# Optimization experiments

Measured on AMD Instinct MI355X. Metric: run time of the kernel, lower is better.

The kernel has to match this reference:

```python
import jax, jax.numpy as jnp
import numpy as np

S, M, B, D, H, DH = 1024, 1024, 4, 1024, 16, 64
T = S + M


def _rel_shift(x):
    # x: [i, j, b, n] -> Transformer-XL relative shift
    i, j = x.shape[0], x.shape[1]
    zero_pad = jnp.zeros((i, 1) + x.shape[2:], x.dtype)
    x_padded = jnp.concatenate([zero_pad, x], axis=1)
    x_padded = x_padded.reshape((j + 1, i) + x.shape[2:])
    return x_padded[1:].reshape(x.shape)


def setup_inputs() -> dict:
    key = jax.random.key(0)
    ks = jax.random.split(key, 8)
    sc = 0.02
    x = jax.random.normal(ks[0], (S, B, D), jnp.float32)
    memory = jax.random.normal(ks[1], (M, B, D), jnp.float32)
    pos_emb = jax.random.normal(ks[2], (T, D), jnp.float32)
    pos_bias_u = jax.random.normal(ks[3], (H, DH), jnp.float32) * sc
    pos_bias_v = jax.random.normal(ks[4], (H, DH), jnp.float32) * sc
    W_qkv = jax.random.normal(ks[5], (D, 3 * H * DH), jnp.float32) * sc
    W_rel = jax.random.normal(ks[6], (D, H * DH), jnp.float32) * sc
    W_o = jax.random.normal(ks[7], (H * DH, D), jnp.float32) * sc
    gamma = jnp.ones((D,), jnp.float32)
    beta = jnp.zeros((D,), jnp.float32)
    # causal mask accounting for memory: query i attends keys j <= i + M
    causal = jnp.arange(T)[None, :] > (jnp.arange(S)[:, None] + M)
    mask = jnp.broadcast_to(causal[:, :, None], (S, T, B))
    return {"x": x, "pos_emb": pos_emb, "pos_bias_u": pos_bias_u,
            "pos_bias_v": pos_bias_v, "memory": memory,
            "W_qkv": W_qkv, "W_rel": W_rel, "W_o": W_o,
            "gamma": gamma, "beta": beta, "mask": mask}


def reference(x, pos_emb, pos_bias_u, pos_bias_v, memory, W_qkv, W_rel, W_o, gamma, beta, mask):
    seq_len, batch, d_model = x.shape
    num_head, d_head = pos_bias_u.shape
    scale = 1.0 / d_head ** 0.5

    c = jnp.concatenate([memory, x], axis=0)          # [T, B, D]
    total_len = c.shape[0]

    qkv = c @ W_qkv                                   # [T, B, 3*H*DH]
    q, k, v = jnp.split(qkv, 3, axis=-1)
    q = q.reshape(total_len, batch, num_head, d_head)[-seq_len:]  # [S,B,H,DH]
    k = k.reshape(total_len, batch, num_head, d_head)             # [T,B,H,DH]
    v = v.reshape(total_len, batch, num_head, d_head)             # [T,B,H,DH]
    r = (pos_emb @ W_rel).reshape(total_len, num_head, d_head)    # [T,H,DH]

    AC = jnp.einsum('ibnd,jbnd->ijbn', q + pos_bias_u, k)  # content-content
    BD = jnp.einsum('ibnd,jnd->ijbn', q + pos_bias_v, r)   # content-position
    BD = _rel_shift(BD)

    attn_score = (AC + BD) * scale                    # [S,T,B,H]
    attn_score = jnp.where(mask[:, :, :, None], -jnp.inf, attn_score)
    attn_prob = jax.nn.softmax(attn_score, axis=1)

    attn_vec = jnp.einsum('ijbn,jbnd->ibnd', attn_prob, v)
    attn_vec = attn_vec.reshape(seq_len, batch, num_head * d_head)
    attn_out = attn_vec @ W_o                         # [S,B,D]

    y = x + attn_out
    mu = jnp.mean(y, axis=-1, keepdims=True)
    var = jnp.var(y, axis=-1, keepdims=True)
    return (y - mu) / jnp.sqrt(var + 1e-5) * gamma + beta
```

## Files before the change

### kernel.cpp

```cpp
#include <hip/hip_runtime.h>
#include <math.h>
#include <cstdint>
#include <cstddef>


typedef _Float16 half_t;
typedef _Float16 half8 __attribute__((ext_vector_type(8)));
typedef _Float16 half4v __attribute__((ext_vector_type(4)));
typedef float f32x4 __attribute__((ext_vector_type(4)));

#define S_LEN 1024
#define M_LEN 1024
#define T_LEN 2048
#define BATCH 4
#define NHEAD 16

__device__ inline void async_copy16(const half_t* g, half_t* l) {
  __builtin_amdgcn_global_load_lds(
      (const __attribute__((address_space(1))) void*)g,
      (__attribute__((address_space(3))) void*)l, 16, 0, 0);
}

__global__ __launch_bounds__(256) void k_convert3(const float* __restrict__ mem,
                                                  const float* __restrict__ x,
                                                  const float* __restrict__ pos,
                                                  half_t* __restrict__ cbf,
                                                  half_t* __restrict__ posb) {
  const int i = blockIdx.x * 256 + threadIdx.x;
  const float* src;
  half_t* dst;
  int off;
  if (i < 1048576)      { src = mem; dst = cbf;           off = i; }
  else if (i < 2097152) { src = x;   dst = cbf + 4194304; off = i - 1048576; }
  else                  { src = pos; dst = posb;          off = i - 2097152; }
  const float4 v = ((const float4*)src)[off];
  half4v h;
  h[0] = (half_t)v.x; h[1] = (half_t)v.y; h[2] = (half_t)v.z; h[3] = (half_t)v.w;
  ((half4v*)dst)[off] = h;
}

__global__ __launch_bounds__(256) void k_transpose_w3(const float* __restrict__ Wqkv,
                                                      const float* __restrict__ Wrel,
                                                      const float* __restrict__ Wo,
                                                      half_t* __restrict__ wqkvT,
                                                      half_t* __restrict__ wrelT,
                                                      half_t* __restrict__ woT) {
  __shared__ float tile[64][65];
  const int y = blockIdx.y;
  const float* src; half_t* dst; int C, c0;
  if (y < 48)      { src = Wqkv; dst = wqkvT; C = 3072; c0 = y * 64; }
  else if (y < 64) { src = Wrel; dst = wrelT; C = 1024; c0 = (y - 48) * 64; }
  else             { src = Wo;   dst = woT;   C = 1024; c0 = (y - 64) * 64; }
  const int t = threadIdx.x;
  const int r0 = blockIdx.x * 64;
  const int tx = t & 63, ty4 = t >> 6;
#pragma unroll
  for (int k = 0; k < 16; ++k) {
    int row = k * 4 + ty4;
    tile[row][tx] = src[(size_t)(r0 + row) * C + c0 + tx];
  }
  __syncthreads();
#pragma unroll
  for (int k = 0; k < 16; ++k) {
    int orow = k * 4 + ty4;
    dst[(size_t)(c0 + orow) * 1024 + r0 + tx] = (half_t)tile[tx][orow];
  }
}

__device__ inline void gemm_body(const half_t* __restrict__ A,
                                 const half_t* __restrict__ B,
                                 half_t* __restrict__ C,
                                 int N, int K, int ld, int m0, int n0,
                                 half_t (*ldsA)[64], half_t (*ldsB)[64]) {
  const int t = threadIdx.x;
  const int wave = t >> 6, lane = t & 63, quad = lane >> 4, l15 = lane & 15;
  const int wm = (wave >> 1) * 64, wn = (wave & 1) * 64;
  const int srow = lane >> 3;
  const int scol = ((lane & 7) ^ srow) * 8;
  f32x4 acc[4][4] = {};
  for (int k0 = 0; k0 < K; k0 += 64) {
    __syncthreads();
#pragma unroll
    for (int i = 0; i < 4; ++i) {
      const int r0 = (wave * 4 + i) * 8;
      async_copy16(&A[(size_t)(m0 + r0 + srow) * ld + k0 + scol], &ldsA[r0][0]);
      async_copy16(&B[(size_t)(n0 + r0 + srow) * ld + k0 + scol], &ldsB[r0][0]);
    }
    __syncthreads();
#pragma unroll
    for (int ks = 0; ks < 2; ++ks) {
      half8 af[4], bf[4];
#pragma unroll
      for (int mt = 0; mt < 4; ++mt)
        af[mt] = *(const half8*)&ldsA[wm + mt * 16 + l15][((ks * 4 + quad) ^ (l15 & 7)) * 8];
#pragma unroll
      for (int nt = 0; nt < 4; ++nt)
        bf[nt] = *(const half8*)&ldsB[wn + nt * 16 + l15][((ks * 4 + quad) ^ (l15 & 7)) * 8];
#pragma unroll
      for (int mt = 0; mt < 4; ++mt)
#pragma unroll
        for (int nt = 0; nt < 4; ++nt)
          acc[mt][nt] = __builtin_amdgcn_mfma_f32_16x16x32_f16(af[mt], bf[nt], acc[mt][nt], 0, 0, 0);
    }
  }
#pragma unroll
  for (int mt = 0; mt < 4; ++mt)
#pragma unroll
    for (int nt = 0; nt < 4; ++nt)
#pragma unroll
      for (int r = 0; r < 4; ++r) {
        const int row = m0 + wm + mt * 16 + quad * 4 + r;
        const int col = n0 + wn + nt * 16 + l15;
        C[(size_t)row * N + col] = (half_t)acc[mt][nt][r];
      }
}

__global__ __launch_bounds__(256) void k_gemm_qkv_pos(const half_t* __restrict__ cbf,
                                                      const half_t* __restrict__ wqkvT,
                                                      half_t* __restrict__ qkv,
                                                      const half_t* __restrict__ posb,
                                                      const half_t* __restrict__ wrelT,
                                                      half_t* __restrict__ rb) {
  __shared__ half_t ldsA[128][64];
  __shared__ half_t ldsB[128][64];
  const int bid = blockIdx.x;
  if (bid < 1536)
    gemm_body(cbf, wqkvT, qkv, 3072, 1024, 1024, (bid & 63) * 128, (bid >> 6) * 128, ldsA, ldsB);
  else {
    const int b2 = bid - 1536;
    gemm_body(posb, wrelT, rb, 1024, 1024, 1024, (b2 & 15) * 128, (b2 >> 4) * 128, ldsA, ldsB);
  }
}

__global__ __launch_bounds__(256) void k_gemm_proj(const half_t* __restrict__ av,
                                                   const half_t* __restrict__ woT,
                                                   half_t* __restrict__ out0,
                                                   half_t* __restrict__ out1) {
  __shared__ half_t ldsA[128][64];
  __shared__ half_t ldsB[128][64];
  const int bid = blockIdx.x;
  const int h = bid >> 8, b2 = bid & 255;
  gemm_body(av + h * 512, woT + h * 512, h ? out1 : out0,
            1024, 512, 1024, (b2 & 31) * 128, (b2 >> 5) * 128, ldsA, ldsB);
}

__global__ __launch_bounds__(256) void k_transpose_v(const half_t* __restrict__ qkv,
                                                     half_t* __restrict__ vT) {
  __shared__ half_t tile[64][72];
  const int t = threadIdx.x;
  const int t0 = blockIdx.x * 64, bn = blockIdx.y, b = bn >> 4, n = bn & 15;
#pragma unroll
  for (int i = 0; i < 2; ++i) {
    const int ci = t + i * 256;
    const int row = ci >> 3, co = (ci & 7) * 8;
    *(half8*)&tile[row][co] =
        *(const half8*)&qkv[((size_t)(t0 + row) * BATCH + b) * 3072 + 2048 + n * 64 + co];
  }
  __syncthreads();
#pragma unroll
  for (int i = 0; i < 2; ++i) {
    const int ci = t + i * 256;
    const int dh = ci >> 3, to = (ci & 7) * 8;
    half8 v;
#pragma unroll
    for (int j = 0; j < 8; ++j) v[j] = tile[to + j][dh];
    *(half8*)&vT[((size_t)bn * 64 + dh) * 2048 + t0 + to] = v;
  }
}

__global__ __launch_bounds__(512, 4) void k_attn(const half_t* __restrict__ qkv,
                                                 const half_t* __restrict__ rbuf,
                                                 const half_t* __restrict__ vT,
                                                 const float* __restrict__ pbu,
                                                 const float* __restrict__ pbv,
                                                 half_t* __restrict__ av) {
  __shared__ __align__(16) half_t ldsK[64][64];
  __shared__ __align__(16) half_t ldsV[64][64];
  __shared__ __align__(16) half_t ldsR[256][64];
  __shared__ __align__(16) half_t ldsP[8][16][72];
  const int t = threadIdx.x;
  const int wave = t >> 6, lane = t & 63, quad = lane >> 4, l15 = lane & 15;

  const int li = blockIdx.x + 8 * blockIdx.y;
  const int c = li & 255, kr = li >> 8;
  const int xe = kr == 0 ? (c & 7) : 7 - (c & 7);
  const int bn = (c >> 3) + (kr << 5);
  const int i0 = xe * 128;
  const int b = bn >> 4, n = bn & 15;
  const int i_base = i0 + wave * 16;
  const int p0 = 896 - i0;

  half8 qu[2], qv[2];
#pragma unroll
  for (int ks = 0; ks < 2; ++ks) {
    const int dh0 = ks * 32 + quad * 8;
    const half8 qf = *(const half8*)&qkv[((size_t)(M_LEN + i_base + l15) * BATCH + b) * 3072 + n * 64 + dh0];
#pragma unroll
    for (int j = 0; j < 8; ++j) {
      const float qj = (float)qf[j];
      qu[ks][j] = (half_t)(qj + pbu[n * 64 + dh0 + j]);
      qv[ks][j] = (half_t)(qj + pbv[n * 64 + dh0 + j]);
    }
  }

  int bperm_idx[4];
  bool lo_sel[4];
#pragma unroll
  for (int r = 0; r < 4; ++r) {
    const int irow = quad * 4 + r;
    bperm_idx[r] = ((lane & 48) | ((l15 + 15 - irow) & 15)) << 2;
    lo_sel[r] = (l15 <= irow);
  }

  f32x4 oacc[4] = {};
  float lpart[4] = {0.f, 0.f, 0.f, 0.f};
  const float k1 = 0.125f * 1.44269504088896f;
  const float kC = -4.0f * 1.44269504088896f;

  const int srow = t >> 3, sc3 = t & 7;
  const int sxk = (sc3 ^ (srow & 7)) * 8;

  const int ntile = xe * 2 + 18;

  half8 kreg = *(const half8*)&qkv[((size_t)srow * BATCH + b) * 3072 + 1024 + n * 64 + sc3 * 8];
  half8 vreg = *(const half8*)&vT[((size_t)bn * 64 + srow) * 2048 + sc3 * 8];
  half8 rreg4[4];
  int rr4[4], rc4[4];
#pragma unroll
  for (int i = 0; i < 4; ++i) {
    const int ci = t + 512 * i;
    rr4[i] = ci >> 3; rc4[i] = ci & 7;
    const int ps = p0 + rr4[i] > 2047 ? 2047 : p0 + rr4[i];
    rreg4[i] = *(const half8*)&rbuf[(size_t)ps * 1024 + n * 64 + rc4[i] * 8];
  }
  half8 rpre;

  for (int kt = 0; kt < ntile; ++kt) {
    const int j0 = kt * 64;

    __syncthreads();
    *(half8*)&ldsK[srow][sxk] = kreg;
    *(half8*)&ldsV[srow][sxk] = vreg;
    if (kt == 0) {
#pragma unroll
      for (int i = 0; i < 4; ++i) {
        const int pg = p0 + rr4[i];
        *(half8*)&ldsR[pg & 255][(rc4[i] ^ (pg & 7)) * 8] = rreg4[i];
      }
    } else {
      const int pw = j0 + p0 + 192 + srow;
      *(half8*)&ldsR[pw & 255][(sc3 ^ (pw & 7)) * 8] = rpre;
    }
    __syncthreads();

    if (kt + 1 < ntile) {
      const int j0n = j0 + 64;
      kreg = *(const half8*)&qkv[((size_t)(j0n + srow) * BATCH + b) * 3072 + 1024 + n * 64 + sc3 * 8];
      vreg = *(const half8*)&vT[((size_t)bn * 64 + srow) * 2048 + j0n + sc3 * 8];
      const int pn = j0 + p0 + 256 + srow;
      const int pc = pn > 2047 ? 2047 : pn;
      rpre = *(const half8*)&rbuf[(size_t)pc * 1024 + n * 64 + sc3 * 8];
    }

    f32x4 ac[4] = {};
#pragma unroll
    for (int ks = 0; ks < 2; ++ks)
#pragma unroll
      for (int nt = 0; nt < 4; ++nt) {
        const int row = nt * 16 + l15;
        const half8 kf = *(const half8*)&ldsK[row][((ks * 4 + quad) ^ (row & 7)) * 8];
        ac[nt] = __builtin_amdgcn_mfma_f32_16x16x32_f16(qu[ks], kf, ac[nt], 0, 0, 0);
      }

    const int rbg = j0 + p0 + 112 - wave * 16;
    f32x4 ea[5] = {};
#pragma unroll
    for (int ks = 0; ks < 2; ++ks)
#pragma unroll
      for (int et = 0; et < 5; ++et) {
        const int pr = rbg + et * 16 + l15;
        const half8 rf = *(const half8*)&ldsR[pr & 255][((ks * 4 + quad) ^ (pr & 7)) * 8];
        ea[et] = __builtin_amdgcn_mfma_f32_16x16x32_f16(qv[ks], rf, ea[et], 0, 0, 0);
      }

    const bool maskt = j0 > i_base + 960;
#pragma unroll
    for (int r = 0; r < 4; ++r) {
      const int irow = quad * 4 + r;
      const int ig = i_base + irow;
      float rot[5];
#pragma unroll
      for (int et = 0; et < 5; ++et)
        rot[et] = __int_as_float(
            __builtin_amdgcn_ds_bpermute(bperm_idx[r], __float_as_int(ea[et][r])));
      float psum = 0.f;
#pragma unroll
      for (int nt = 0; nt < 4; ++nt) {
        const float ev = lo_sel[r] ? rot[nt] : rot[nt + 1];
        const int cj = nt * 16 + l15;
        float p = __builtin_amdgcn_exp2f(fmaf(ac[nt][r] + ev, k1, kC));
        if (maskt && (j0 + cj > ig + M_LEN)) p = 0.f;
        psum += p;
        ldsP[wave][irow][cj] = (half_t)p;
      }
      lpart[r] += psum;
    }
    __builtin_amdgcn_wave_barrier();

    half8 pa[2];
#pragma unroll
    for (int ks = 0; ks < 2; ++ks)
      pa[ks] = *(const half8*)&ldsP[wave][l15][ks * 32 + quad * 8];
#pragma unroll
    for (int ks = 0; ks < 2; ++ks)
#pragma unroll
      for (int dnt = 0; dnt < 4; ++dnt) {
        const int row = dnt * 16 + l15;
        const half8 vf = *(const half8*)&ldsV[row][((ks * 4 + quad) ^ (row & 7)) * 8];
        oacc[dnt] = __builtin_amdgcn_mfma_f32_16x16x32_f16(pa[ks], vf, oacc[dnt], 0, 0, 0);
      }
  }

#pragma unroll
  for (int r = 0; r < 4; ++r) {
    float l = lpart[r];
#pragma unroll
    for (int off = 1; off < 16; off <<= 1) l += __shfl_xor(l, off);
    const float inv = 1.0f / l;
    const int ig = i_base + quad * 4 + r;
#pragma unroll
    for (int dnt = 0; dnt < 4; ++dnt)
      av[((size_t)ig * BATCH + b) * 1024 + n * 64 + dnt * 16 + l15] = (half_t)(oacc[dnt][r] * inv);
  }
}

__global__ __launch_bounds__(256) void k_ln(const float* __restrict__ x,
                                            const half_t* __restrict__ ao0,
                                            const half_t* __restrict__ ao1,
                                            const float* __restrict__ gamma,
                                            const float* __restrict__ beta,
                                            float* __restrict__ out) {
  const int row = blockIdx.x;
  const int t = threadIdx.x;
  const float4 xv = ((const float4*)(x + (size_t)row * 1024))[t];
  const half4v a4 = ((const half4v*)(ao0 + (size_t)row * 1024))[t];
  const half4v b4 = ((const half4v*)(ao1 + (size_t)row * 1024))[t];
  const float y0 = xv.x + (float)a4[0] + (float)b4[0];
  const float y1 = xv.y + (float)a4[1] + (float)b4[1];
  const float y2 = xv.z + (float)a4[2] + (float)b4[2];
  const float y3 = xv.w + (float)a4[3] + (float)b4[3];
  float s = y0 + y1 + y2 + y3;
  float ss = y0 * y0 + y1 * y1 + y2 * y2 + y3 * y3;
#pragma unroll
  for (int off = 1; off < 64; off <<= 1) {
    s += __shfl_xor(s, off);
    ss += __shfl_xor(ss, off);
  }
  __shared__ float sb[4], ssb[4];
  if ((t & 63) == 0) { sb[t >> 6] = s; ssb[t >> 6] = ss; }
  __syncthreads();
  s = sb[0] + sb[1] + sb[2] + sb[3];
  ss = ssb[0] + ssb[1] + ssb[2] + ssb[3];
  const float mean = s * (1.f / 1024.f);
  const float var = ss * (1.f / 1024.f) - mean * mean;
  const float rstd = rsqrtf(var + 1e-5f);
  const float4 g = ((const float4*)gamma)[t];
  const float4 be = ((const float4*)beta)[t];
  float4 o;
  o.x = (y0 - mean) * rstd * g.x + be.x;
  o.y = (y1 - mean) * rstd * g.y + be.y;
  o.z = (y2 - mean) * rstd * g.z + be.z;
  o.w = (y3 - mean) * rstd * g.w + be.w;
  ((float4*)(out + (size_t)row * 1024))[t] = o;
}

extern "C" void kernel_launch(void* const* d_in, const int* in_sizes, int n_in,
                              void* d_out, int out_size, void* d_ws, size_t ws_size,
                              hipStream_t stream) {
  const float* x     = (const float*)d_in[0];
  const float* pos   = (const float*)d_in[1];
  const float* pbu   = (const float*)d_in[2];
  const float* pbv   = (const float*)d_in[3];
  const float* mem   = (const float*)d_in[4];
  const float* Wqkv  = (const float*)d_in[5];
  const float* Wrel  = (const float*)d_in[6];
  const float* Wo    = (const float*)d_in[7];
  const float* gamma = (const float*)d_in[8];
  const float* beta  = (const float*)d_in[9];
  float* out = (float*)d_out;

  half_t* ws    = (half_t*)d_ws;
  half_t* cbf   = ws;
  half_t* posb  = cbf + 8388608;
  half_t* wqkvT = posb + 2097152;
  half_t* wrelT = wqkvT + 3145728;
  half_t* woT   = wrelT + 1048576;
  half_t* qkv   = woT + 1048576;
  half_t* rb    = qkv + 25165824;
  half_t* vT    = rb + 2097152;
  half_t* av    = vT + 8388608;
  half_t* aout0 = qkv;
  half_t* aout1 = qkv + 4194304;

  k_convert3<<<10240, 256, 0, stream>>>(mem, x, pos, cbf, posb);
  k_transpose_w3<<<dim3(16, 80), 256, 0, stream>>>(Wqkv, Wrel, Wo, wqkvT, wrelT, woT);
  k_gemm_qkv_pos<<<1664, 256, 0, stream>>>(cbf, wqkvT, qkv, posb, wrelT, rb);
  k_transpose_v<<<dim3(32, 64), 256, 0, stream>>>(qkv, vT);
  k_attn<<<dim3(8, 64), 512, 0, stream>>>(qkv, rb, vT, pbu, pbv, av);
  k_gemm_proj<<<512, 256, 0, stream>>>(av, woT, aout0, aout1);
  k_ln<<<4096, 256, 0, stream>>>(x, aout0, aout1, gamma, beta, out);
}
```

Before: 333.4 us.

## Split attention key range into two balanced passes per block with combine kernel

Each attention block now handles two query tiles instead of one. It processes the first half of the key range for query tile kq and the second half for query tile 7-kq, so every block runs the same number of key tiles. This removes the causal-length imbalance between blocks. Because the softmax uses a fixed offset rather than a running max, partial outputs and row sums can be written unnormalized and added in a new small combine kernel. The cost is extra global writes and reads for the partial results, one more kernel launch, and a second Q/R prologue per block.

```diff
diff --git a/kernel.cpp b/kernel.cpp
--- a/kernel.cpp
+++ b/kernel.cpp
@@ -173,7 +173,9 @@
                                                  const half_t* __restrict__ vT,
                                                  const float* __restrict__ pbu,
                                                  const float* __restrict__ pbv,
-                                                 half_t* __restrict__ av) {
+                                                 half_t* __restrict__ av0,
+                                                 half_t* __restrict__ av1,
+                                                 float* __restrict__ lsum) {
   __shared__ __align__(16) half_t ldsK[64][64];
   __shared__ __align__(16) half_t ldsV[64][64];
   __shared__ __align__(16) half_t ldsR[256][64];
@@ -182,26 +184,9 @@
   const int wave = t >> 6, lane = t & 63, quad = lane >> 4, l15 = lane & 15;
 
   const int li = blockIdx.x + 8 * blockIdx.y;
-  const int c = li & 255, kr = li >> 8;
-  const int xe = kr == 0 ? (c & 7) : 7 - (c & 7);
-  const int bn = (c >> 3) + (kr << 5);
-  const int i0 = xe * 128;
+  const int kq = li & 7;
+  const int bn = li >> 3;
   const int b = bn >> 4, n = bn & 15;
-  const int i_base = i0 + wave * 16;
-  const int p0 = 896 - i0;
-
-  half8 qu[2], qv[2];
-#pragma unroll
-  for (int ks = 0; ks < 2; ++ks) {
-    const int dh0 = ks * 32 + quad * 8;
-    const half8 qf = *(const half8*)&qkv[((size_t)(M_LEN + i_base + l15) * BATCH + b) * 3072 + n * 64 + dh0];
-#pragma unroll
-    for (int j = 0; j < 8; ++j) {
-      const float qj = (float)qf[j];
-      qu[ks][j] = (half_t)(qj + pbu[n * 64 + dh0 + j]);
-      qv[ks][j] = (half_t)(qj + pbv[n * 64 + dh0 + j]);
-    }
-  }
 
   int bperm_idx[4];
   bool lo_sel[4];
@@ -212,126 +197,167 @@
     lo_sel[r] = (l15 <= irow);
   }
 
-  f32x4 oacc[4] = {};
-  float lpart[4] = {0.f, 0.f, 0.f, 0.f};
   const float k1 = 0.125f * 1.44269504088896f;
   const float kC = -4.0f * 1.44269504088896f;
 
   const int srow = t >> 3, sc3 = t & 7;
   const int sxk = (sc3 ^ (srow & 7)) * 8;
 
-  const int ntile = xe * 2 + 18;
-
-  half8 kreg = *(const half8*)&qkv[((size_t)srow * BATCH + b) * 3072 + 1024 + n * 64 + sc3 * 8];
-  half8 vreg = *(const half8*)&vT[((size_t)bn * 64 + srow) * 2048 + sc3 * 8];
-  half8 rreg4[4];
-  int rr4[4], rc4[4];
-#pragma unroll
-  for (int i = 0; i < 4; ++i) {
-    const int ci = t + 512 * i;
-    rr4[i] = ci >> 3; rc4[i] = ci & 7;
-    const int ps = p0 + rr4[i] > 2047 ? 2047 : p0 + rr4[i];
-    rreg4[i] = *(const half8*)&rbuf[(size_t)ps * 1024 + n * 64 + rc4[i] * 8];
-  }
-  half8 rpre;
-
-  for (int kt = 0; kt < ntile; ++kt) {
-    const int j0 = kt * 64;
-
-    __syncthreads();
-    *(half8*)&ldsK[srow][sxk] = kreg;
-    *(half8*)&ldsV[srow][sxk] = vreg;
-    if (kt == 0) {
-#pragma unroll
-      for (int i = 0; i < 4; ++i) {
-        const int pg = p0 + rr4[i];
-        *(half8*)&ldsR[pg & 255][(rc4[i] ^ (pg & 7)) * 8] = rreg4[i];
+  for (int pass = 0; pass < 2; ++pass) {
+    const int xe = pass ? 7 - kq : kq;
+    const int i0 = xe * 128;
+    const int i_base = i0 + wave * 16;
+    const int p0 = 896 - i0;
+    const int kt0 = pass ? xe + 9 : 0;
+    const int kt1 = pass ? 2 * xe + 18 : xe + 9;
+
+    half8 qu[2], qv[2];
+#pragma unroll
+    for (int ks = 0; ks < 2; ++ks) {
+      const int dh0 = ks * 32 + quad * 8;
+      const half8 qf = *(const half8*)&qkv[((size_t)(M_LEN + i_base + l15) * BATCH + b) * 3072 + n * 64 + dh0];
+#pragma unroll
+      for (int j = 0; j < 8; ++j) {
+        const float qj = (float)qf[j];
+        qu[ks][j] = (half_t)(qj + pbu[n * 64 + dh0 + j]);
+        qv[ks][j] = (half_t)(qj + pbv[n * 64 + dh0 + j]);
       }
-    } else {
-      const int pw = j0 + p0 + 192 + srow;
-      *(half8*)&ldsR[pw & 255][(sc3 ^ (pw & 7)) * 8] = rpre;
-    }
-    __syncthreads();
-
-    if (kt + 1 < ntile) {
-      const int j0n = j0 + 64;
-      kreg = *(const half8*)&qkv[((size_t)(j0n + srow) * BATCH + b) * 3072 + 1024 + n * 64 + sc3 * 8];
-      vreg = *(const half8*)&vT[((size_t)bn * 64 + srow) * 2048 + j0n + sc3 * 8];
-      const int pn = j0 + p0 + 256 + srow;
-      const int pc = pn > 2047 ? 2047 : pn;
-      rpre = *(const half8*)&rbuf[(size_t)pc * 1024 + n * 64 + sc3 * 8];
-    }
-
-    f32x4 ac[4] = {};
-#pragma unroll
-    for (int ks = 0; ks < 2; ++ks)
-#pragma unroll
-      for (int nt = 0; nt < 4; ++nt) {
-        const int row = nt * 16 + l15;
-        const half8 kf = *(const half8*)&ldsK[row][((ks * 4 + quad) ^ (row & 7)) * 8];
-        ac[nt] = __builtin_amdgcn_mfma_f32_16x16x32_f16(qu[ks], kf, ac[nt], 0, 0, 0);
+    }
+
+    f32x4 oacc[4] = {};
+    float lpart[4] = {0.f, 0.f, 0.f, 0.f};
+
+    const int jb = kt0 * 64;
+    half8 kreg = *(const half8*)&qkv[((size_t)(jb + srow) * BATCH + b) * 3072 + 1024 + n * 64 + sc3 * 8];
+    half8 vreg = *(const half8*)&vT[((size_t)bn * 64 + srow) * 2048 + jb + sc3 * 8];
+    half8 rreg4[4];
+    int rr4[4], rc4[4];
+#pragma unroll
+    for (int i = 0; i < 4; ++i) {
+      const int ci = t + 512 * i;
+      rr4[i] = ci >> 3; rc4[i] = ci & 7;
+      const int pg = p0 + jb + rr4[i];
+      const int ps = pg > 2047 ? 2047 : pg;
+      rreg4[i] = *(const half8*)&rbuf[(size_t)ps * 1024 + n * 64 + rc4[i] * 8];
+    }
+    half8 rpre;
+
+    for (int kt = kt0; kt < kt1; ++kt) {
+      const int j0 = kt * 64;
+
+      __syncthreads();
+      *(half8*)&ldsK[srow][sxk] = kreg;
+      *(half8*)&ldsV[srow][sxk] = vreg;
+      if (kt == kt0) {
+#pragma unroll
+        for (int i = 0; i < 4; ++i) {
+          const int pg = p0 + jb + rr4[i];
+          *(half8*)&ldsR[pg & 255][(rc4[i] ^ (pg & 7)) * 8] = rreg4[i];
+        }
+      } else {
+        const int pw = j0 + p0 + 192 + srow;
+        *(half8*)&ldsR[pw & 255][(sc3 ^ (pw & 7)) * 8] = rpre;
       }
-
-    const int rbg = j0 + p0 + 112 - wave * 16;
-    f32x4 ea[5] = {};
-#pragma unroll
-    for (int ks = 0; ks < 2; ++ks)
-#pragma unroll
-      for (int et = 0; et < 5; ++et) {
-        const int pr = rbg + et * 16 + l15;
-        const half8 rf = *(const half8*)&ldsR[pr & 255][((ks * 4 + quad) ^ (pr & 7)) * 8];
-        ea[et] = __builtin_amdgcn_mfma_f32_16x16x32_f16(qv[ks], rf, ea[et], 0, 0, 0);
+      __syncthreads();
+
+      if (kt + 1 < kt1) {
+        const int j0n = j0 + 64;
+        kreg = *(const half8*)&qkv[((size_t)(j0n + srow) * BATCH + b) * 3072 + 1024 + n * 64 + sc3 * 8];
+        vreg = *(const half8*)&vT[((size_t)bn * 64 + srow) * 2048 + j0n + sc3 * 8];
+        const int pn = j0 + p0 + 256 + srow;
+        const int pc = pn > 2047 ? 2047 : pn;
+        rpre = *(const half8*)&rbuf[(size_t)pc * 1024 + n * 64 + sc3 * 8];
       }
 
-    const bool maskt = j0 > i_base + 960;
+      f32x4 ac[4] = {};
+#pragma unroll
+      for (int ks = 0; ks < 2; ++ks)
+#pragma unroll
+        for (int nt = 0; nt < 4; ++nt) {
+          const int row = nt * 16 + l15;
+          const half8 kf = *(const half8*)&ldsK[row][((ks * 4 + quad) ^ (row & 7)) * 8];
+          ac[nt] = __builtin_amdgcn_mfma_f32_16x16x32_f16(qu[ks], kf, ac[nt], 0, 0, 0);
+        }
+
+      const int rbg = j0 + p0 + 112 - wave * 16;
+      f32x4 ea[5] = {};
+#pragma unroll
+      for (int ks = 0; ks < 2; ++ks)
+#pragma unroll
+        for (int et = 0; et < 5; ++et) {
+          const int pr = rbg + et * 16 + l15;
+          const half8 rf = *(const half8*)&ldsR[pr & 255][((ks * 4 + quad) ^ (pr & 7)) * 8];
+          ea[et] = __builtin_amdgcn_mfma_f32_16x16x32_f16(qv[ks], rf, ea[et], 0, 0, 0);
+        }
+
+      const bool maskt = j0 > i_base + 960;
+#pragma unroll
+      for (int r = 0; r < 4; ++r) {
+        const int irow = quad * 4 + r;
+        const int ig = i_base + irow;
+        float rot[5];
+#pragma unroll
+        for (int et = 0; et < 5; ++et)
+          rot[et] = __int_as_float(
+              __builtin_amdgcn_ds_bpermute(bperm_idx[r], __float_as_int(ea[et][r])));
+        float psum = 0.f;
+#pragma unroll
+        for (int nt = 0; nt < 4; ++nt) {
+          const float ev = lo_sel[r] ? rot[nt] : rot[nt + 1];
+          const int cj = nt * 16 + l15;
+          float p = __builtin_amdgcn_exp2f(fmaf(ac[nt][r] + ev, k1, kC));
+          if (maskt && (j0 + cj > ig + M_LEN)) p = 0.f;
+          psum += p;
+          ldsP[wave][irow][cj] = (half_t)p;
+        }
+        lpart[r] += psum;
+      }
+      __builtin_amdgcn_wave_barrier();
+
+      half8 pa[2];
+#pragma unroll
+      for (int ks = 0; ks < 2; ++ks)
+        pa[ks] = *(const half8*)&ldsP[wave][l15][ks * 32 + quad * 8];
+#pragma unroll
+      for (int ks = 0; ks < 2; ++ks)
+#pragma unroll
+        for (int dnt = 0; dnt < 4; ++dnt) {
+          const int row = dnt * 16 + l15;
+          const half8 vf = *(const half8*)&ldsV[row][((ks * 4 + quad) ^ (row & 7)) * 8];
+          oacc[dnt] = __builtin_amdgcn_mfma_f32_16x16x32_f16(pa[ks], vf, oacc[dnt], 0, 0, 0);
+        }
+    }
+
+    half_t* __restrict__ avh = pass ? av1 : av0;
+    float* __restrict__ lb = lsum + (pass ? 65536 : 0);
 #pragma unroll
     for (int r = 0; r < 4; ++r) {
-      const int irow = quad * 4 + r;
-      const int ig = i_base + irow;
-      float rot[5];
-#pragma unroll
-      for (int et = 0; et < 5; ++et)
-        rot[et] = __int_as_float(
-            __builtin_amdgcn_ds_bpermute(bperm_idx[r], __float_as_int(ea[et][r])));
-      float psum = 0.f;
-#pragma unroll
-      for (int nt = 0; nt < 4; ++nt) {
-        const float ev = lo_sel[r] ? rot[nt] : rot[nt + 1];
-        const int cj = nt * 16 + l15;
-        float p = __builtin_amdgcn_exp2f(fmaf(ac[nt][r] + ev, k1, kC));
-        if (maskt && (j0 + cj > ig + M_LEN)) p = 0.f;
-        psum += p;
-        ldsP[wave][irow][cj] = (half_t)p;
-      }
-      lpart[r] += psum;
-    }
-    __builtin_amdgcn_wave_barrier();
-
-    half8 pa[2];
-#pragma unroll
-    for (int ks = 0; ks < 2; ++ks)
-      pa[ks] = *(const half8*)&ldsP[wave][l15][ks * 32 + quad * 8];
-#pragma unroll
-    for (int ks = 0; ks < 2; ++ks)
-#pragma unroll
-      for (int dnt = 0; dnt < 4; ++dnt) {
-        const int row = dnt * 16 + l15;
-        const half8 vf = *(const half8*)&ldsV[row][((ks * 4 + quad) ^ (row & 7)) * 8];
-        oacc[dnt] = __builtin_amdgcn_mfma_f32_16x16x32_f16(pa[ks], vf, oacc[dnt], 0, 0, 0);
-      }
-  }
-
-#pragma unroll
-  for (int r = 0; r < 4; ++r) {
-    float l = lpart[r];
-#pragma unroll
-    for (int off = 1; off < 16; off <<= 1) l += __shfl_xor(l, off);
-    const float inv = 1.0f / l;
-    const int ig = i_base + quad * 4 + r;
-#pragma unroll
-    for (int dnt = 0; dnt < 4; ++dnt)
-      av[((size_t)ig * BATCH + b) * 1024 + n * 64 + dnt * 16 + l15] = (half_t)(oacc[dnt][r] * inv);
-  }
+      float l = lpart[r];
+#pragma unroll
+      for (int off = 1; off < 16; off <<= 1) l += __shfl_xor(l, off);
+      const int ig = i_base + quad * 4 + r;
+#pragma unroll
+      for (int dnt = 0; dnt < 4; ++dnt)
+        avh[((size_t)ig * BATCH + b) * 1024 + n * 64 + dnt * 16 + l15] = (half_t)oacc[dnt][r];
+      if (l15 == 0) lb[((size_t)ig * BATCH + b) * 16 + n] = l;
+    }
+  }
+}
+
+__global__ __launch_bounds__(256) void k_combine(const half_t* __restrict__ a0,
+                                                 const half_t* __restrict__ a1,
+                                                 const float* __restrict__ lsum,
+                                                 half_t* __restrict__ av) {
+  const int row = blockIdx.x;
+  const int t = threadIdx.x;
+  const int n = t >> 4;
+  const float inv = 1.f / (lsum[row * 16 + n] + lsum[65536 + row * 16 + n]);
+  const half4v x0 = ((const half4v*)(a0 + (size_t)row * 1024))[t];
+  const half4v x1 = ((const half4v*)(a1 + (size_t)row * 1024))[t];
+  half4v o;
+#pragma unroll
+  for (int j = 0; j < 4; ++j) o[j] = (half_t)(((float)x0[j] + (float)x1[j]) * inv);
+  ((half4v*)(av + (size_t)row * 1024))[t] = o;
 }
 
 __global__ __launch_bounds__(256) void k_ln(const float* __restrict__ x,
@@ -401,12 +427,16 @@
   half_t* av    = vT + 8388608;
   half_t* aout0 = qkv;
   half_t* aout1 = qkv + 4194304;
+  half_t* av0c  = cbf;
+  half_t* av1c  = posb;
+  float*  lsum  = (float*)wrelT;
 
   k_convert3<<<10240, 256, 0, stream>>>(mem, x, pos, cbf, posb);
   k_transpose_w3<<<dim3(16, 80), 256, 0, stream>>>(Wqkv, Wrel, Wo, wqkvT, wrelT, woT);
   k_gemm_qkv_pos<<<1664, 256, 0, stream>>>(cbf, wqkvT, qkv, posb, wrelT, rb);
   k_transpose_v<<<dim3(32, 64), 256, 0, stream>>>(qkv, vT);
-  k_attn<<<dim3(8, 64), 512, 0, stream>>>(qkv, rb, vT, pbu, pbv, av);
+  k_attn<<<dim3(8, 64), 512, 0, stream>>>(qkv, rb, vT, pbu, pbv, av0c, av1c, lsum);
+  k_combine<<<4096, 256, 0, stream>>>(av0c, av1c, lsum, av);
   k_gemm_proj<<<512, 256, 0, stream>>>(av, woT, aout0, aout1);
   k_ln<<<4096, 256, 0, stream>>>(x, aout0, aout1, gamma, beta, out);
 }
```

Result: slower. 356.5 us (+6.9%).

## Software-pipeline attention tiles by overlapping next-tile scores with current softmax/PV

Applied to the files above, without the earlier changes.

Splits the attention loop into stage, prefetch, compute-scores and finish (exp, mask, P·V) phases. The loop is unrolled by two so that the QK/QR MFMAs of tile kt+1 are issued before the softmax and PV of tile kt. V is double-buffered in LDS so that both tiles' data stay live. s_setprio raises wave priority around the MFMA blocks to help interleave matrix and VALU/exp work across waves. The cost is extra LDS, extra score registers per thread, and an odd-even loop structure that relies on the tile count being even.

```diff
diff --git a/kernel.cpp b/kernel.cpp
--- a/kernel.cpp
+++ b/kernel.cpp
@@ -175,7 +175,7 @@
                                                  const float* __restrict__ pbv,
                                                  half_t* __restrict__ av) {
   __shared__ __align__(16) half_t ldsK[64][64];
-  __shared__ __align__(16) half_t ldsV[64][64];
+  __shared__ __align__(16) half_t ldsV[2][64][64];
   __shared__ __align__(16) half_t ldsR[256][64];
   __shared__ __align__(16) half_t ldsP[8][16][72];
   const int t = threadIdx.x;
@@ -214,6 +214,7 @@
 
   f32x4 oacc[4] = {};
   float lpart[4] = {0.f, 0.f, 0.f, 0.f};
+  float sA[4][4], sB[4][4];
   const float k1 = 0.125f * 1.44269504088896f;
   const float kC = -4.0f * 1.44269504088896f;
 
@@ -235,12 +236,10 @@
   }
   half8 rpre;
 
-  for (int kt = 0; kt < ntile; ++kt) {
-    const int j0 = kt * 64;
-
+  auto STAGE = [&](int kt, int par) {
     __syncthreads();
     *(half8*)&ldsK[srow][sxk] = kreg;
-    *(half8*)&ldsV[srow][sxk] = vreg;
+    *(half8*)&ldsV[par][srow][sxk] = vreg;
     if (kt == 0) {
 #pragma unroll
       for (int i = 0; i < 4; ++i) {
@@ -248,20 +247,26 @@
         *(half8*)&ldsR[pg & 255][(rc4[i] ^ (pg & 7)) * 8] = rreg4[i];
       }
     } else {
-      const int pw = j0 + p0 + 192 + srow;
+      const int pw = kt * 64 + p0 + 192 + srow;
       *(half8*)&ldsR[pw & 255][(sc3 ^ (pw & 7)) * 8] = rpre;
     }
     __syncthreads();
-
-    if (kt + 1 < ntile) {
-      const int j0n = j0 + 64;
+  };
+
+  auto PREFETCH = [&](int ktn) {
+    if (ktn < ntile) {
+      const int j0n = ktn * 64;
       kreg = *(const half8*)&qkv[((size_t)(j0n + srow) * BATCH + b) * 3072 + 1024 + n * 64 + sc3 * 8];
       vreg = *(const half8*)&vT[((size_t)bn * 64 + srow) * 2048 + j0n + sc3 * 8];
-      const int pn = j0 + p0 + 256 + srow;
+      const int pn = j0n + p0 + 192 + srow;
       const int pc = pn > 2047 ? 2047 : pn;
       rpre = *(const half8*)&rbuf[(size_t)pc * 1024 + n * 64 + sc3 * 8];
     }
-
+  };
+
+  auto COMPUTE = [&](int kt, float (&S)[4][4]) {
+    const int j0 = kt * 64;
+    __builtin_amdgcn_s_setprio(1);
     f32x4 ac[4] = {};
 #pragma unroll
     for (int ks = 0; ks < 2; ++ks)
@@ -271,7 +276,6 @@
         const half8 kf = *(const half8*)&ldsK[row][((ks * 4 + quad) ^ (row & 7)) * 8];
         ac[nt] = __builtin_amdgcn_mfma_f32_16x16x32_f16(qu[ks], kf, ac[nt], 0, 0, 0);
       }
-
     const int rbg = j0 + p0 + 112 - wave * 16;
     f32x4 ea[5] = {};
 #pragma unroll
@@ -282,44 +286,66 @@
         const half8 rf = *(const half8*)&ldsR[pr & 255][((ks * 4 + quad) ^ (pr & 7)) * 8];
         ea[et] = __builtin_amdgcn_mfma_f32_16x16x32_f16(qv[ks], rf, ea[et], 0, 0, 0);
       }
-
-    const bool maskt = j0 > i_base + 960;
+    __builtin_amdgcn_s_setprio(0);
+#pragma unroll
+    for (int r = 0; r < 4; ++r) {
+      float rot[5];
+#pragma unroll
+      for (int et = 0; et < 5; ++et)
+        rot[et] = __int_as_float(
+            __builtin_amdgcn_ds_bpermute(bperm_idx[r], __float_as_int(ea[et][r])));
+#pragma unroll
+      for (int nt = 0; nt < 4; ++nt)
+        S[r][nt] = ac[nt][r] + (lo_sel[r] ? rot[nt] : rot[nt + 1]);
+    }
+  };
+
+  auto FINISH = [&](int ktp, float (&S)[4][4], int par) {
+    const int j0p = ktp * 64;
+    const bool maskt = j0p > i_base + 960;
 #pragma unroll
     for (int r = 0; r < 4; ++r) {
       const int irow = quad * 4 + r;
       const int ig = i_base + irow;
-      float rot[5];
-#pragma unroll
-      for (int et = 0; et < 5; ++et)
-        rot[et] = __int_as_float(
-            __builtin_amdgcn_ds_bpermute(bperm_idx[r], __float_as_int(ea[et][r])));
       float psum = 0.f;
 #pragma unroll
       for (int nt = 0; nt < 4; ++nt) {
-        const float ev = lo_sel[r] ? rot[nt] : rot[nt + 1];
         const int cj = nt * 16 + l15;
-        float p = __builtin_amdgcn_exp2f(fmaf(ac[nt][r] + ev, k1, kC));
-        if (maskt && (j0 + cj > ig + M_LEN)) p = 0.f;
+        float p = __builtin_amdgcn_exp2f(fmaf(S[r][nt], k1, kC));
+        if (maskt && (j0p + cj > ig + M_LEN)) p = 0.f;
         psum += p;
         ldsP[wave][irow][cj] = (half_t)p;
       }
       lpart[r] += psum;
     }
     __builtin_amdgcn_wave_barrier();
-
     half8 pa[2];
 #pragma unroll
     for (int ks = 0; ks < 2; ++ks)
       pa[ks] = *(const half8*)&ldsP[wave][l15][ks * 32 + quad * 8];
+    __builtin_amdgcn_s_setprio(1);
 #pragma unroll
     for (int ks = 0; ks < 2; ++ks)
 #pragma unroll
       for (int dnt = 0; dnt < 4; ++dnt) {
         const int row = dnt * 16 + l15;
-        const half8 vf = *(const half8*)&ldsV[row][((ks * 4 + quad) ^ (row & 7)) * 8];
+        const half8 vf = *(const half8*)&ldsV[par][row][((ks * 4 + quad) ^ (row & 7)) * 8];
         oacc[dnt] = __builtin_amdgcn_mfma_f32_16x16x32_f16(pa[ks], vf, oacc[dnt], 0, 0, 0);
       }
-  }
+    __builtin_amdgcn_s_setprio(0);
+  };
+
+  for (int kt = 0; kt < ntile; kt += 2) {
+    STAGE(kt, 0);
+    PREFETCH(kt + 1);
+    COMPUTE(kt, sA);
+    if (kt > 0) FINISH(kt - 1, sB, 1);
+    STAGE(kt + 1, 1);
+    PREFETCH(kt + 2);
+    COMPUTE(kt + 1, sB);
+    FINISH(kt, sA, 0);
+  }
+  FINISH(ntile - 1, sB, 1);
 
 #pragma unroll
   for (int r = 0; r < 4; ++r) {
```

After: 457.2 us. 37.1% more time.

## Use 256x256 double-buffered tiles with XOR swizzle in QKV/pos GEMM

Applied to the files above, without the earlier changes.

Replaces the shared 128x128 gemm_body path for the QKV and positional projections with a dedicated kernel. It uses 256x256 tiles, 512 threads and double-buffered async global-to-LDS loads that overlap the next K-slice with MFMA compute. LDS is XOR-swizzled to avoid bank conflicts, and block IDs are remapped to group blocks across XCDs. The larger tiles raise data reuse per block, at the cost of 128-float accumulators per thread (register pressure) and 64KB of LDS per block, which limits occupancy.

```diff
diff --git a/kernel.cpp b/kernel.cpp
--- a/kernel.cpp
+++ b/kernel.cpp
@@ -115,21 +115,84 @@
       }
 }
 
-__global__ __launch_bounds__(256) void k_gemm_qkv_pos(const half_t* __restrict__ cbf,
-                                                      const half_t* __restrict__ wqkvT,
-                                                      half_t* __restrict__ qkv,
-                                                      const half_t* __restrict__ posb,
-                                                      const half_t* __restrict__ wrelT,
-                                                      half_t* __restrict__ rb) {
-  __shared__ half_t ldsA[128][64];
-  __shared__ half_t ldsB[128][64];
-  const int bid = blockIdx.x;
-  if (bid < 1536)
-    gemm_body(cbf, wqkvT, qkv, 3072, 1024, 1024, (bid & 63) * 128, (bid >> 6) * 128, ldsA, ldsB);
-  else {
-    const int b2 = bid - 1536;
-    gemm_body(posb, wrelT, rb, 1024, 1024, 1024, (b2 & 15) * 128, (b2 >> 4) * 128, ldsA, ldsB);
-  }
+#define QP_STAGE(buf_, k0_)                                                    \
+  do {                                                                         \
+    _Pragma("unroll") for (int i_ = 0; i_ < 4; ++i_) {                         \
+      const int r0_ = wave * 32 + i_ * 8;                                      \
+      async_copy16(&A[(size_t)(m0 + r0_ + srw) * 1024 + (k0_) + scl],          \
+                   &ldsA[buf_][r0_][0]);                                       \
+      async_copy16(&B[(size_t)(n0 + r0_ + srw) * 1024 + (k0_) + scl],          \
+                   &ldsB[buf_][r0_][0]);                                       \
+    }                                                                          \
+  } while (0)
+
+#define QP_COMPUTE(d_)                                                         \
+  do {                                                                         \
+    _Pragma("unroll") for (int ks_ = 0; ks_ < 2; ++ks_) {                      \
+      half8 bf_[4];                                                            \
+      _Pragma("unroll") for (int nt_ = 0; nt_ < 4; ++nt_) {                    \
+        const int rw_ = wn + nt_ * 16 + l15;                                   \
+        bf_[nt_] =                                                             \
+            *(const half8*)&ldsB[d_][rw_][((ks_ * 4 + quad) ^ (rw_ & 7)) * 8]; \
+      }                                                                        \
+      half8 af_[8];                                                            \
+      _Pragma("unroll") for (int mt_ = 0; mt_ < 8; ++mt_) {                    \
+        const int rw_ = wm + mt_ * 16 + l15;                                   \
+        af_[mt_] =                                                             \
+            *(const half8*)&ldsA[d_][rw_][((ks_ * 4 + quad) ^ (rw_ & 7)) * 8]; \
+      }                                                                        \
+      __builtin_amdgcn_s_setprio(1);                                           \
+      _Pragma("unroll") for (int mt_ = 0; mt_ < 8; ++mt_)                      \
+        _Pragma("unroll") for (int nt_ = 0; nt_ < 4; ++nt_)                    \
+          acc[mt_][nt_] = __builtin_amdgcn_mfma_f32_16x16x32_f16(              \
+              af_[mt_], bf_[nt_], acc[mt_][nt_], 0, 0, 0);                     \
+      __builtin_amdgcn_s_setprio(0);                                           \
+    }                                                                          \
+  } while (0)
+
+__global__ __launch_bounds__(512, 2) void k_gemm_qkv_pos(const half_t* __restrict__ cbf,
+                                                         const half_t* __restrict__ wqkvT,
+                                                         half_t* __restrict__ qkv,
+                                                         const half_t* __restrict__ posb,
+                                                         const half_t* __restrict__ wrelT,
+                                                         half_t* __restrict__ rb) {
+  __shared__ half_t ldsA[2][256][64];
+  __shared__ half_t ldsB[2][256][64];
+  const int t = threadIdx.x;
+  const int wave = t >> 6, lane = t & 63, quad = lane >> 4, l15 = lane & 15;
+  const int bid0 = blockIdx.x;
+  const int bid = (bid0 & 7) * 52 + (bid0 >> 3);
+  const half_t* A; const half_t* B; half_t* C; int m0, n0, N;
+  if (bid < 384) { A = cbf;  B = wqkvT; C = qkv; N = 3072;
+                   m0 = (bid & 31) * 256; n0 = (bid >> 5) * 256; }
+  else { const int b2 = bid - 384;
+         A = posb; B = wrelT; C = rb;  N = 1024;
+         m0 = (b2 & 7) * 256; n0 = (b2 >> 3) * 256; }
+  const int srw = lane >> 3;
+  const int scl = ((lane & 7) ^ srw) * 8;
+  const int wm = (wave >> 2) * 128, wn = (wave & 3) * 64;
+
+  f32x4 acc[8][4] = {};
+
+  QP_STAGE(0, 0);
+  __syncthreads();
+  int d = 0;
+  for (int kt = 0; kt < 15; ++kt) {
+    QP_STAGE(d ^ 1, (kt + 1) * 64);
+    QP_COMPUTE(d);
+    __syncthreads();
+    d ^= 1;
+  }
+  QP_COMPUTE(d);
+
+#pragma unroll
+  for (int mt = 0; mt < 8; ++mt)
+#pragma unroll
+    for (int nt = 0; nt < 4; ++nt)
+#pragma unroll
+      for (int r = 0; r < 4; ++r)
+        C[(size_t)(m0 + wm + mt * 16 + quad * 4 + r) * N + n0 + wn + nt * 16 + l15] =
+            (half_t)acc[mt][nt][r];
 }
 
 __global__ __launch_bounds__(256) void k_gemm_proj(const half_t* __restrict__ av,
@@ -404,7 +467,7 @@
 
   k_convert3<<<10240, 256, 0, stream>>>(mem, x, pos, cbf, posb);
   k_transpose_w3<<<dim3(16, 80), 256, 0, stream>>>(Wqkv, Wrel, Wo, wqkvT, wrelT, woT);
-  k_gemm_qkv_pos<<<1664, 256, 0, stream>>>(cbf, wqkvT, qkv, posb, wrelT, rb);
+  k_gemm_qkv_pos<<<416, 512, 0, stream>>>(cbf, wqkvT, qkv, posb, wrelT, rb);
   k_transpose_v<<<dim3(32, 64), 256, 0, stream>>>(qkv, vT);
   k_attn<<<dim3(8, 64), 512, 0, stream>>>(qkv, rb, vT, pbu, pbv, av);
   k_gemm_proj<<<512, 256, 0, stream>>>(av, woT, aout0, aout1);
```

After: 330.5 us. Within noise of the previous version (-0.9%).
